# Kernel optimization log

Measured on AMD Instinct MI355X. Metric: run time of the kernel, lower is better.

## Reference

```python
import jax, jax.numpy as jnp
import numpy as np

TAU = 0.07        # temperature from init_kwargs
EPS = 1e-8        # torch F.cosine_similarity eps
NEG_INF = -1e9    # mask fill value used by the original module


def setup_inputs() -> dict:
    key = jax.random.key(0)
    k1, k2 = jax.random.split(key)
    B, D = 4096, 512
    anchor = jax.random.normal(k1, (B, D), dtype=jnp.float32)
    positive = jax.random.normal(k2, (B, D), dtype=jnp.float32)
    return {"anchor": anchor, "positive": positive}


def reference(anchor, positive):
    B = anchor.shape[0]
    N = 2 * B
    emb = jnp.concatenate([anchor, positive], axis=0)          # (2B, D)
    # cosine similarity matrix == normalized dot products (same math as the
    # broadcasted F.cosine_similarity, without the O(N^2 D) intermediate)
    norm = jnp.maximum(jnp.linalg.norm(emb, axis=1, keepdims=True), EPS)
    z = emb / norm
    sim = jnp.matmul(z, z.T) / TAU                             # (2B, 2B)

    idx = jnp.arange(N)
    pos_idx = (idx + B) % N                                    # positive pair index
    pos_logits = sim[idx, pos_idx][:, None]                    # (2B, 1)

    # negatives: everything except self and the positive pair
    neg_mask = (
        jnp.ones((N, N), dtype=bool)
        .at[idx, idx].set(False)
        .at[idx, pos_idx].set(False)
    )
    neg_logits = jnp.where(neg_mask, sim, NEG_INF)             # (2B, 2B)

    all_logits = jnp.concatenate([pos_logits, neg_logits], axis=1)  # (2B, 2B+1)
    loss_per_sample = -pos_logits[:, 0] + jax.scipy.special.logsumexp(all_logits, axis=1)
    # every row has a positive, so valid_samples is all-True; reduction='mean'
    return loss_per_sample.mean()
```

## Files before the change

### kernel.cpp

```cpp
#include <hip/hip_runtime.h>
#include <hip/hip_bf16.h>
#include <stdint.h>


#define N_TOT   8192
#define B_HALF  4096
#define DDIM    512
#define INV_TAU 14.285714285714286f
#define TTILES  32
#define NKT     16

typedef __bf16 bf16x8 __attribute__((ext_vector_type(8)));
typedef __bf16 bf16x4 __attribute__((ext_vector_type(4)));
typedef float  floatx4 __attribute__((ext_vector_type(4)));

__device__ __forceinline__ void gl2lds16(const void* g, void* l) {
    __builtin_amdgcn_global_load_lds(
        (const __attribute__((address_space(1))) void*)g,
        (__attribute__((address_space(3))) void*)l, 16, 0, 0);
}

#define S_BARRIER() asm volatile("s_barrier" ::: "memory")
#define LGKM0()     do { asm volatile("s_waitcnt lgkmcnt(0)" ::: "memory"); \
                         __builtin_amdgcn_sched_barrier(0); } while (0)
#define VMCNT4()    asm volatile("s_waitcnt vmcnt(4)" ::: "memory")
#define VMCNT0()    asm volatile("s_waitcnt vmcnt(0)" ::: "memory")
#define VM_NONE()   do {} while (0)

__global__ __launch_bounds__(256) void knorm(const float* __restrict__ anchor,
                                             const float* __restrict__ positive,
                                             __bf16* __restrict__ z,
                                             float* __restrict__ row_sums,
                                             float* __restrict__ out) {
    const int row  = blockIdx.x * 4 + (threadIdx.x >> 6);
    const int lane = threadIdx.x & 63;
    if (lane == 0) row_sums[row] = 0.0f;
    if (blockIdx.x == 0 && threadIdx.x == 0) out[0] = 0.0f;
    const float* src = (row < B_HALF) ? (anchor + (size_t)row * DDIM)
                                      : (positive + (size_t)(row - B_HALF) * DDIM);
    float4 v0 = ((const float4*)src)[lane];
    float4 v1 = ((const float4*)src)[lane + 64];
    float ss = v0.x*v0.x + v0.y*v0.y + v0.z*v0.z + v0.w*v0.w
             + v1.x*v1.x + v1.y*v1.y + v1.z*v1.z + v1.w*v1.w;
    #pragma unroll
    for (int m = 1; m < 64; m <<= 1) ss += __shfl_xor(ss, m, 64);
    const float inv = 1.0f / fmaxf(sqrtf(ss), 1e-8f);
    bf16x4 o0, o1;
    o0[0] = (__bf16)(v0.x*inv); o0[1] = (__bf16)(v0.y*inv);
    o0[2] = (__bf16)(v0.z*inv); o0[3] = (__bf16)(v0.w*inv);
    o1[0] = (__bf16)(v1.x*inv); o1[1] = (__bf16)(v1.y*inv);
    o1[2] = (__bf16)(v1.z*inv); o1[3] = (__bf16)(v1.w*inv);
    bf16x4* dst = (bf16x4*)(z + (size_t)row * DDIM);
    dst[lane]      = o0;
    dst[lane + 64] = o1;
}

__global__ __launch_bounds__(512, 2) void ksim(const __bf16* __restrict__ z,
                                               float* __restrict__ row_sums,
                                               float* __restrict__ pos_sims) {
    int bid = (int)blockIdx.x;
    bid = (bid & 7) * 66 + (bid >> 3);
    int rem = bid, rt = 0;
    while (rem >= TTILES - rt) { rem -= TTILES - rt; rt++; }
    const int ct = rt + rem;
    const bool diag = (rt == ct);
    const bool posb = (ct == rt + 16);

    const int r0 = rt * 256, c0 = ct * 256;
    const int tid  = threadIdx.x;
    const int w    = tid >> 6, lane = tid & 63;
    const int quad = lane >> 4, nlo = lane & 15;
    const int wr   = w >> 2,   wc  = w & 3;
    const int s4   = (nlo >> 1) & 3;

    __shared__ __align__(16) char smem[4][32768];

    const int schunk = ((lane & 3) ^ ((lane >> 3) & 3)) * 8;
    const __bf16* zA = z + (size_t)(r0 + w * 16 + (lane >> 2)) * DDIM + schunk;
    const __bf16* zB = z + (size_t)(c0 + w * 16 + (lane >> 2)) * DDIM + schunk;

#define STAGE_A(T2) do { char* s_ = smem[(T2) & 3]; const int kb_ = (T2) * 32;   \
        gl2lds16(zA + kb_,              s_ + w * 1024);                          \
        gl2lds16(zA + 128 * DDIM + kb_, s_ + 8192 + w * 1024); } while (0)
#define STAGE_B(T2) do { char* s_ = smem[(T2) & 3]; const int kb_ = (T2) * 32;   \
        gl2lds16(zB + kb_,              s_ + 16384 + w * 1024);                  \
        gl2lds16(zB + 128 * DDIM + kb_, s_ + 16384 + 8192 + w * 1024); } while (0)

    floatx4 acc[8][4];
    #pragma unroll
    for (int a = 0; a < 8; a++)
        #pragma unroll
        for (int b = 0; b < 4; b++) acc[a][b] = (floatx4){0.f, 0.f, 0.f, 0.f};

    STAGE_A(0); STAGE_B(0);
    STAGE_A(1); STAGE_B(1);
    VMCNT4();
    S_BARRIER();

#define KTILE(T, DO_STAGE, VMW) do {                                                  \
        char* As_ = smem[(T) & 3];                                                    \
        char* Bs_ = As_ + 16384;                                                      \
        bf16x8 af[4], bfr[4];                                                         \
                                                    \
        _Pragma("unroll") for (int mi = 0; mi < 4; mi++)                              \
            af[mi] = *(const bf16x8*)(As_ + (wr * 128 + mi * 16 + nlo) * 64           \
                                          + ((quad ^ s4) * 16));                      \
        _Pragma("unroll") for (int ni = 0; ni < 4; ni++)                              \
            bfr[ni] = *(const bf16x8*)(Bs_ + (wc * 64 + ni * 16 + nlo) * 64           \
                                           + ((quad ^ s4) * 16));                     \
        if (DO_STAGE) STAGE_A((T) + 2);                                               \
        S_BARRIER(); LGKM0();                                                         \
        __builtin_amdgcn_s_setprio(1);                                                \
        _Pragma("unroll") for (int mi = 0; mi < 4; mi++)                              \
            _Pragma("unroll") for (int ni = 0; ni < 4; ni++)                          \
                acc[mi][ni] = __builtin_amdgcn_mfma_f32_16x16x32_bf16(                \
                    af[mi], bfr[ni], acc[mi][ni], 0, 0, 0);                           \
        __builtin_amdgcn_s_setprio(0);                                                \
        S_BARRIER();                                                                  \
                           \
        _Pragma("unroll") for (int mi = 0; mi < 4; mi++)                              \
            af[mi] = *(const bf16x8*)(As_ + (wr * 128 + 64 + mi * 16 + nlo) * 64      \
                                          + ((quad ^ s4) * 16));                      \
        if (DO_STAGE) STAGE_B((T) + 2);                                               \
        S_BARRIER(); LGKM0();                                                         \
        __builtin_amdgcn_s_setprio(1);                                                \
        _Pragma("unroll") for (int mi = 0; mi < 4; mi++)                              \
            _Pragma("unroll") for (int ni = 0; ni < 4; ni++)                          \
                acc[4 + mi][ni] = __builtin_amdgcn_mfma_f32_16x16x32_bf16(            \
                    af[mi], bfr[ni], acc[4 + mi][ni], 0, 0, 0);                       \
        __builtin_amdgcn_s_setprio(0);                                                \
        VMW();                                                                        \
        S_BARRIER();                                                                  \
    } while (0)

    for (int t = 0; t < NKT - 2; ++t) KTILE(t, true, VMCNT4);
    KTILE(NKT - 2, false, VMCNT0);
    KTILE(NKT - 1, false, VM_NONE);

    __syncthreads();
    float* rbuf = (float*)smem;
    float* cbuf = (float*)(smem[0] + 4096);

    float cs[4] = {0.f, 0.f, 0.f, 0.f};
    #pragma unroll
    for (int mi = 0; mi < 8; mi++) {
        #pragma unroll
        for (int reg = 0; reg < 4; reg++) {
            const int il = wr * 128 + mi * 16 + quad * 4 + reg;
            const int i  = r0 + il;
            const int ipos = i ^ B_HALF;
            float rs = 0.f;
            #pragma unroll
            for (int ni = 0; ni < 4; ni++) {
                const int j = c0 + wc * 64 + ni * 16 + nlo;
                const float sim = acc[mi][ni][reg] * INV_TAU;
                float e = __expf(sim - INV_TAU);
                if (diag && j == i) e = 0.f;
                if (posb && j == ipos) {
                    pos_sims[i] = sim;
                    pos_sims[j] = sim;
                }
                rs += e;
                cs[ni] += e;
            }
            rs += __shfl_xor(rs, 1, 64);
            rs += __shfl_xor(rs, 2, 64);
            rs += __shfl_xor(rs, 4, 64);
            rs += __shfl_xor(rs, 8, 64);
            if (nlo == 0) rbuf[il * 4 + wc] = rs;
        }
    }
    if (!diag) {
        #pragma unroll
        for (int ni = 0; ni < 4; ni++) {
            float c = cs[ni];
            c += __shfl_xor(c, 16, 64);
            c += __shfl_xor(c, 32, 64);
            if (quad == 0) cbuf[(wc * 64 + ni * 16 + nlo) * 2 + wr] = c;
        }
    }
    __syncthreads();
    if (tid < 256) {
        const float s = rbuf[tid * 4] + rbuf[tid * 4 + 1]
                      + rbuf[tid * 4 + 2] + rbuf[tid * 4 + 3];
        atomicAdd(&row_sums[r0 + tid], s);
    } else if (!diag) {
        const int c = tid - 256;
        atomicAdd(&row_sums[c0 + c], cbuf[c * 2] + cbuf[c * 2 + 1]);
    }
#undef KTILE
#undef STAGE_A
#undef STAGE_B
}

__global__ __launch_bounds__(256) void kfinal(const float* __restrict__ row_sums,
                                              const float* __restrict__ pos_sims,
                                              float* __restrict__ out) {
    const int r = blockIdx.x * 256 + threadIdx.x;
    float v = INV_TAU + __logf(row_sums[r]) - pos_sims[r];
    #pragma unroll
    for (int m = 1; m < 64; m <<= 1) v += __shfl_xor(v, m, 64);
    __shared__ float wsum[4];
    if ((threadIdx.x & 63) == 0) wsum[threadIdx.x >> 6] = v;
    __syncthreads();
    if (threadIdx.x == 0)
        atomicAdd(out, (wsum[0] + wsum[1] + wsum[2] + wsum[3]) * (1.0f / (float)N_TOT));
}

extern "C" void kernel_launch(void* const* d_in, const int* in_sizes, int n_in,
                              void* d_out, int out_size, void* d_ws, size_t ws_size,
                              hipStream_t stream) {
    const float* anchor   = (const float*)d_in[0];
    const float* positive = (const float*)d_in[1];
    float* out = (float*)d_out;

    char* ws = (char*)d_ws;
    __bf16* z        = (__bf16*)ws;
    float*  row_sums = (float*)(ws + 8388608);
    float*  pos_sims = (float*)(ws + 8388608 + 32768);

    knorm<<<N_TOT / 4, 256, 0, stream>>>(anchor, positive, z, row_sums, out);
    ksim<<<528, 512, 0, stream>>>(z, row_sums, pos_sims);
    kfinal<<<N_TOT / 256, 256, 0, stream>>>(row_sums, pos_sims, out);
}
```

Baseline: 137.5 us.

## Double-buffer LDS fragments, deepen prefetch, and fuse final reduction via last-block counter

Restructures the GEMM main loop to prefetch the next k-tile's A/B register fragments while the current MFMAs run, using partial lgkmcnt waits and one barrier per tile instead of several, and staging three tiles ahead in the 4-slot LDS ring. It also removes the separate kfinal launch by having the last finishing ksim block, detected with an atomic done counter, compute the log-sum loss reduction. This cuts barrier stalls and one kernel launch, at the cost of more register pressure from the extra fragment buffers and a serial final reduction in one block.

```diff
diff --git a/kernel.cpp b/kernel.cpp
--- a/kernel.cpp
+++ b/kernel.cpp
@@ -21,8 +21,6 @@
 }
 
 #define S_BARRIER() asm volatile("s_barrier" ::: "memory")
-#define LGKM0()     do { asm volatile("s_waitcnt lgkmcnt(0)" ::: "memory"); \
-                         __builtin_amdgcn_sched_barrier(0); } while (0)
 #define VMCNT4()    asm volatile("s_waitcnt vmcnt(4)" ::: "memory")
 #define VMCNT0()    asm volatile("s_waitcnt vmcnt(0)" ::: "memory")
 #define VM_NONE()   do {} while (0)
@@ -31,11 +29,11 @@
                                              const float* __restrict__ positive,
                                              __bf16* __restrict__ z,
                                              float* __restrict__ row_sums,
-                                             float* __restrict__ out) {
+                                             unsigned* __restrict__ done_ctr) {
     const int row  = blockIdx.x * 4 + (threadIdx.x >> 6);
     const int lane = threadIdx.x & 63;
     if (lane == 0) row_sums[row] = 0.0f;
-    if (blockIdx.x == 0 && threadIdx.x == 0) out[0] = 0.0f;
+    if (blockIdx.x == 0 && threadIdx.x == 0) *done_ctr = 0u;
     const float* src = (row < B_HALF) ? (anchor + (size_t)row * DDIM)
                                       : (positive + (size_t)(row - B_HALF) * DDIM);
     float4 v0 = ((const float4*)src)[lane];
@@ -57,7 +55,9 @@
 
 __global__ __launch_bounds__(512, 2) void ksim(const __bf16* __restrict__ z,
                                                float* __restrict__ row_sums,
-                                               float* __restrict__ pos_sims) {
+                                               float* __restrict__ pos_sims,
+                                               unsigned* __restrict__ done_ctr,
+                                               float* __restrict__ out) {
     int bid = (int)blockIdx.x;
     bid = (bid & 7) * 66 + (bid >> 3);
     int rem = bid, rt = 0;
@@ -74,6 +74,8 @@
     const int s4   = (nlo >> 1) & 3;
 
     __shared__ __align__(16) char smem[4][32768];
+    __shared__ unsigned lastf;
+    __shared__ float fsum[8];
 
     const int schunk = ((lane & 3) ^ ((lane >> 3) & 3)) * 8;
     const __bf16* zA = z + (size_t)(r0 + w * 16 + (lane >> 2)) * DDIM + schunk;
@@ -92,50 +94,73 @@
         #pragma unroll
         for (int b = 0; b < 4; b++) acc[a][b] = (floatx4){0.f, 0.f, 0.f, 0.f};
 
+    bf16x8 afX[4], afY[4], afH[4], bfX[4], bfY[4];
+    const char* smb = (const char*)smem;
+    const int xo   = (quad ^ s4) * 16;
+    const int aoff = (wr * 128 + nlo) * 64 + xo;
+    const int boff = 16384 + (wc * 64 + nlo) * 64 + xo;
+
     STAGE_A(0); STAGE_B(0);
     STAGE_A(1); STAGE_B(1);
+    STAGE_A(2); STAGE_B(2);
     VMCNT4();
     S_BARRIER();
-
-#define KTILE(T, DO_STAGE, VMW) do {                                                  \
-        char* As_ = smem[(T) & 3];                                                    \
-        char* Bs_ = As_ + 16384;                                                      \
-        bf16x8 af[4], bfr[4];                                                         \
-                                                    \
-        _Pragma("unroll") for (int mi = 0; mi < 4; mi++)                              \
-            af[mi] = *(const bf16x8*)(As_ + (wr * 128 + mi * 16 + nlo) * 64           \
-                                          + ((quad ^ s4) * 16));                      \
-        _Pragma("unroll") for (int ni = 0; ni < 4; ni++)                              \
-            bfr[ni] = *(const bf16x8*)(Bs_ + (wc * 64 + ni * 16 + nlo) * 64           \
-                                           + ((quad ^ s4) * 16));                     \
-        if (DO_STAGE) STAGE_A((T) + 2);                                               \
-        S_BARRIER(); LGKM0();                                                         \
-        __builtin_amdgcn_s_setprio(1);                                                \
-        _Pragma("unroll") for (int mi = 0; mi < 4; mi++)                              \
-            _Pragma("unroll") for (int ni = 0; ni < 4; ni++)                          \
-                acc[mi][ni] = __builtin_amdgcn_mfma_f32_16x16x32_bf16(                \
-                    af[mi], bfr[ni], acc[mi][ni], 0, 0, 0);                           \
-        __builtin_amdgcn_s_setprio(0);                                                \
-        S_BARRIER();                                                                  \
-                           \
-        _Pragma("unroll") for (int mi = 0; mi < 4; mi++)                              \
-            af[mi] = *(const bf16x8*)(As_ + (wr * 128 + 64 + mi * 16 + nlo) * 64      \
-                                          + ((quad ^ s4) * 16));                      \
-        if (DO_STAGE) STAGE_B((T) + 2);                                               \
-        S_BARRIER(); LGKM0();                                                         \
-        __builtin_amdgcn_s_setprio(1);                                                \
-        _Pragma("unroll") for (int mi = 0; mi < 4; mi++)                              \
-            _Pragma("unroll") for (int ni = 0; ni < 4; ni++)                          \
-                acc[4 + mi][ni] = __builtin_amdgcn_mfma_f32_16x16x32_bf16(            \
-                    af[mi], bfr[ni], acc[4 + mi][ni], 0, 0, 0);                       \
-        __builtin_amdgcn_s_setprio(0);                                                \
-        VMW();                                                                        \
-        S_BARRIER();                                                                  \
+    #pragma unroll
+    for (int mi = 0; mi < 4; mi++)
+        afX[mi] = *(const bf16x8*)(smb + aoff + mi * 1024);
+    #pragma unroll
+    for (int ni = 0; ni < 4; ni++)
+        bfX[ni] = *(const bf16x8*)(smb + boff + ni * 1024);
+
+#define TILE(T, AC, AN, BC, BN, DO_STAGE, ISSUE_NEXT, VMW) do {                        \
+        const int sl_ = ((T) & 3) * 32768, sn_ = (((T) + 1) & 3) * 32768;              \
+        _Pragma("unroll") for (int mi = 0; mi < 4; mi++)                               \
+            afH[mi] = *(const bf16x8*)(smb + sl_ + aoff + 4096 + mi * 1024);           \
+        if (DO_STAGE) { STAGE_A((T) + 3); }                                            \
+        asm volatile("s_waitcnt lgkmcnt(4)" ::: "memory");                             \
+        __builtin_amdgcn_sched_barrier(0);                                             \
+        __builtin_amdgcn_s_setprio(1);                                                 \
+        _Pragma("unroll") for (int mi = 0; mi < 4; mi++)                               \
+            _Pragma("unroll") for (int ni = 0; ni < 4; ni++)                           \
+                acc[mi][ni] = __builtin_amdgcn_mfma_f32_16x16x32_bf16(                 \
+                    AC[mi], BC[ni], acc[mi][ni], 0, 0, 0);                             \
+        __builtin_amdgcn_s_setprio(0);                                                 \
+        if (ISSUE_NEXT) {                                                              \
+            _Pragma("unroll") for (int mi = 0; mi < 4; mi++)                           \
+                AN[mi] = *(const bf16x8*)(smb + sn_ + aoff + mi * 1024);               \
+            _Pragma("unroll") for (int ni = 0; ni < 4; ni++)                           \
+                BN[ni] = *(const bf16x8*)(smb + sn_ + boff + ni * 1024);               \
+        }                                                                              \
+        if (DO_STAGE) { STAGE_B((T) + 3); }                                            \
+        if (ISSUE_NEXT) { asm volatile("s_waitcnt lgkmcnt(8)" ::: "memory"); }         \
+        else            { asm volatile("s_waitcnt lgkmcnt(0)" ::: "memory"); }         \
+        __builtin_amdgcn_sched_barrier(0);                                             \
+        __builtin_amdgcn_s_setprio(1);                                                 \
+        _Pragma("unroll") for (int mi = 0; mi < 4; mi++)                               \
+            _Pragma("unroll") for (int ni = 0; ni < 4; ni++)                           \
+                acc[4 + mi][ni] = __builtin_amdgcn_mfma_f32_16x16x32_bf16(             \
+                    afH[mi], BC[ni], acc[4 + mi][ni], 0, 0, 0);                        \
+        __builtin_amdgcn_s_setprio(0);                                                 \
+        VMW();                                                                         \
+        S_BARRIER();                                                                   \
     } while (0)
 
-    for (int t = 0; t < NKT - 2; ++t) KTILE(t, true, VMCNT4);
-    KTILE(NKT - 2, false, VMCNT0);
-    KTILE(NKT - 1, false, VM_NONE);
+    TILE( 0, afX, afY, bfX, bfY, 1, 1, VMCNT4);
+    TILE( 1, afY, afX, bfY, bfX, 1, 1, VMCNT4);
+    TILE( 2, afX, afY, bfX, bfY, 1, 1, VMCNT4);
+    TILE( 3, afY, afX, bfY, bfX, 1, 1, VMCNT4);
+    TILE( 4, afX, afY, bfX, bfY, 1, 1, VMCNT4);
+    TILE( 5, afY, afX, bfY, bfX, 1, 1, VMCNT4);
+    TILE( 6, afX, afY, bfX, bfY, 1, 1, VMCNT4);
+    TILE( 7, afY, afX, bfY, bfX, 1, 1, VMCNT4);
+    TILE( 8, afX, afY, bfX, bfY, 1, 1, VMCNT4);
+    TILE( 9, afY, afX, bfY, bfX, 1, 1, VMCNT4);
+    TILE(10, afX, afY, bfX, bfY, 1, 1, VMCNT4);
+    TILE(11, afY, afX, bfY, bfX, 1, 1, VMCNT4);
+    TILE(12, afX, afY, bfX, bfY, 1, 1, VMCNT4);
+    TILE(13, afY, afX, bfY, bfX, 0, 1, VMCNT0);
+    TILE(14, afX, afY, bfX, bfY, 0, 1, VM_NONE);
+    TILE(15, afY, afX, bfY, bfX, 0, 0, VM_NONE);
 
     __syncthreads();
     float* rbuf = (float*)smem;
@@ -188,23 +213,28 @@
         const int c = tid - 256;
         atomicAdd(&row_sums[c0 + c], cbuf[c * 2] + cbuf[c * 2 + 1]);
     }
-#undef KTILE
+
+    __threadfence();
+    __syncthreads();
+    if (tid == 0) lastf = (atomicAdd(done_ctr, 1u) == 527u) ? 1u : 0u;
+    __syncthreads();
+    if (!lastf) return;
+    __threadfence();
+    float a = 0.f;
+    for (int i = tid; i < N_TOT; i += 512)
+        a += INV_TAU + __logf(row_sums[i]) - pos_sims[i];
+    #pragma unroll
+    for (int m = 1; m < 64; m <<= 1) a += __shfl_xor(a, m, 64);
+    if (lane == 0) fsum[w] = a;
+    __syncthreads();
+    if (tid == 0) {
+        float t = fsum[0] + fsum[1] + fsum[2] + fsum[3]
+                + fsum[4] + fsum[5] + fsum[6] + fsum[7];
+        out[0] = t * (1.0f / (float)N_TOT);
+    }
+#undef TILE
 #undef STAGE_A
 #undef STAGE_B
-}
-
-__global__ __launch_bounds__(256) void kfinal(const float* __restrict__ row_sums,
-                                              const float* __restrict__ pos_sims,
-                                              float* __restrict__ out) {
-    const int r = blockIdx.x * 256 + threadIdx.x;
-    float v = INV_TAU + __logf(row_sums[r]) - pos_sims[r];
-    #pragma unroll
-    for (int m = 1; m < 64; m <<= 1) v += __shfl_xor(v, m, 64);
-    __shared__ float wsum[4];
-    if ((threadIdx.x & 63) == 0) wsum[threadIdx.x >> 6] = v;
-    __syncthreads();
-    if (threadIdx.x == 0)
-        atomicAdd(out, (wsum[0] + wsum[1] + wsum[2] + wsum[3]) * (1.0f / (float)N_TOT));
 }
 
 extern "C" void kernel_launch(void* const* d_in, const int* in_sizes, int n_in,
@@ -218,8 +248,8 @@
     __bf16* z        = (__bf16*)ws;
     float*  row_sums = (float*)(ws + 8388608);
     float*  pos_sims = (float*)(ws + 8388608 + 32768);
-
-    knorm<<<N_TOT / 4, 256, 0, stream>>>(anchor, positive, z, row_sums, out);
-    ksim<<<528, 512, 0, stream>>>(z, row_sums, pos_sims);
-    kfinal<<<N_TOT / 256, 256, 0, stream>>>(row_sums, pos_sims, out);
-}
+    unsigned* done_ctr = (unsigned*)(ws + 8388608 + 65536);
+
+    knorm<<<N_TOT / 4, 256, 0, stream>>>(anchor, positive, z, row_sums, done_ctr);
+    ksim<<<528, 512, 0, stream>>>(z, row_sums, pos_sims, done_ctr, out);
+}
```

Result: slower. 200.3 us (+45.6%).

## Replace LDS-pipelined 256x256 sim tiles with direct-global-load 128x128 tiles

Applied to the files above, without the earlier changes.

The similarity kernel drops the LDS staging pipeline (global_load_lds, barriers, swizzle) and has each wave read MFMA operands straight from global memory. Output tiles shrink from 256x256 to 128x128 on 4-wave blocks, so the launch grows from 528 to 2080 blocks. Per-row and per-column partial sums are now atomically added from each wave rather than reduced in shared memory first. The aim is to cut synchronization overhead and improve load balance. The cost is losing LDS data reuse, which raises global/L2 traffic, plus many more atomics.

```diff
diff --git a/kernel.cpp b/kernel.cpp
--- a/kernel.cpp
+++ b/kernel.cpp
@@ -7,25 +7,11 @@
 #define B_HALF  4096
 #define DDIM    512
 #define INV_TAU 14.285714285714286f
-#define TTILES  32
-#define NKT     16
+#define TTILES  64
 
 typedef __bf16 bf16x8 __attribute__((ext_vector_type(8)));
 typedef __bf16 bf16x4 __attribute__((ext_vector_type(4)));
 typedef float  floatx4 __attribute__((ext_vector_type(4)));
-
-__device__ __forceinline__ void gl2lds16(const void* g, void* l) {
-    __builtin_amdgcn_global_load_lds(
-        (const __attribute__((address_space(1))) void*)g,
-        (__attribute__((address_space(3))) void*)l, 16, 0, 0);
-}
-
-#define S_BARRIER() asm volatile("s_barrier" ::: "memory")
-#define LGKM0()     do { asm volatile("s_waitcnt lgkmcnt(0)" ::: "memory"); \
-                         __builtin_amdgcn_sched_barrier(0); } while (0)
-#define VMCNT4()    asm volatile("s_waitcnt vmcnt(4)" ::: "memory")
-#define VMCNT0()    asm volatile("s_waitcnt vmcnt(0)" ::: "memory")
-#define VM_NONE()   do {} while (0)
 
 __global__ __launch_bounds__(256) void knorm(const float* __restrict__ anchor,
                                              const float* __restrict__ positive,
@@ -55,142 +41,106 @@
     dst[lane + 64] = o1;
 }
 
-__global__ __launch_bounds__(512, 2) void ksim(const __bf16* __restrict__ z,
+__global__ __launch_bounds__(256, 3) void ksim(const __bf16* __restrict__ z,
                                                float* __restrict__ row_sums,
                                                float* __restrict__ pos_sims) {
     int bid = (int)blockIdx.x;
-    bid = (bid & 7) * 66 + (bid >> 3);
+    bid = (bid & 7) * 260 + (bid >> 3);
     int rem = bid, rt = 0;
     while (rem >= TTILES - rt) { rem -= TTILES - rt; rt++; }
     const int ct = rt + rem;
     const bool diag = (rt == ct);
-    const bool posb = (ct == rt + 16);
+    const bool posb = (ct == rt + 32);
 
-    const int r0 = rt * 256, c0 = ct * 256;
+    const int r0 = rt * 128, c0 = ct * 128;
     const int tid  = threadIdx.x;
     const int w    = tid >> 6, lane = tid & 63;
     const int quad = lane >> 4, nlo = lane & 15;
-    const int wr   = w >> 2,   wc  = w & 3;
-    const int s4   = (nlo >> 1) & 3;
+    const int wrow = (w >> 1) * 64, wcol = (w & 1) * 64;
 
-    __shared__ __align__(16) char smem[4][32768];
+    const __bf16* pa = z + (size_t)(r0 + wrow + nlo) * DDIM + quad * 8;
+    const __bf16* pb = z + (size_t)(c0 + wcol + nlo) * DDIM + quad * 8;
 
-    const int schunk = ((lane & 3) ^ ((lane >> 3) & 3)) * 8;
-    const __bf16* zA = z + (size_t)(r0 + w * 16 + (lane >> 2)) * DDIM + schunk;
-    const __bf16* zB = z + (size_t)(c0 + w * 16 + (lane >> 2)) * DDIM + schunk;
-
-#define STAGE_A(T2) do { char* s_ = smem[(T2) & 3]; const int kb_ = (T2) * 32;   \
-        gl2lds16(zA + kb_,              s_ + w * 1024);                          \
-        gl2lds16(zA + 128 * DDIM + kb_, s_ + 8192 + w * 1024); } while (0)
-#define STAGE_B(T2) do { char* s_ = smem[(T2) & 3]; const int kb_ = (T2) * 32;   \
-        gl2lds16(zB + kb_,              s_ + 16384 + w * 1024);                  \
-        gl2lds16(zB + 128 * DDIM + kb_, s_ + 16384 + 8192 + w * 1024); } while (0)
-
-    floatx4 acc[8][4];
+    floatx4 acc[4][4];
     #pragma unroll
-    for (int a = 0; a < 8; a++)
+    for (int a = 0; a < 4; a++)
         #pragma unroll
         for (int b = 0; b < 4; b++) acc[a][b] = (floatx4){0.f, 0.f, 0.f, 0.f};
 
-    STAGE_A(0); STAGE_B(0);
-    STAGE_A(1); STAGE_B(1);
-    VMCNT4();
-    S_BARRIER();
+    #pragma unroll 4
+    for (int kt = 0; kt < 16; kt++) {
+        bf16x8 af[4], bfr[4];
+        #pragma unroll
+        for (int mi = 0; mi < 4; mi++)
+            af[mi] = *(const bf16x8*)(pa + mi * 16 * DDIM + kt * 32);
+        #pragma unroll
+        for (int ni = 0; ni < 4; ni++)
+            bfr[ni] = *(const bf16x8*)(pb + ni * 16 * DDIM + kt * 32);
+        #pragma unroll
+        for (int mi = 0; mi < 4; mi++)
+            #pragma unroll
+            for (int ni = 0; ni < 4; ni++)
+                acc[mi][ni] = __builtin_amdgcn_mfma_f32_16x16x32_bf16(
+                    af[mi], bfr[ni], acc[mi][ni], 0, 0, 0);
+    }
 
-#define KTILE(T, DO_STAGE, VMW) do {                                                  \
-        char* As_ = smem[(T) & 3];                                                    \
-        char* Bs_ = As_ + 16384;                                                      \
-        bf16x8 af[4], bfr[4];                                                         \
-                                                    \
-        _Pragma("unroll") for (int mi = 0; mi < 4; mi++)                              \
-            af[mi] = *(const bf16x8*)(As_ + (wr * 128 + mi * 16 + nlo) * 64           \
-                                          + ((quad ^ s4) * 16));                      \
-        _Pragma("unroll") for (int ni = 0; ni < 4; ni++)                              \
-            bfr[ni] = *(const bf16x8*)(Bs_ + (wc * 64 + ni * 16 + nlo) * 64           \
-                                           + ((quad ^ s4) * 16));                     \
-        if (DO_STAGE) STAGE_A((T) + 2);                                               \
-        S_BARRIER(); LGKM0();                                                         \
-        __builtin_amdgcn_s_setprio(1);                                                \
-        _Pragma("unroll") for (int mi = 0; mi < 4; mi++)                              \
-            _Pragma("unroll") for (int ni = 0; ni < 4; ni++)                          \
-                acc[mi][ni] = __builtin_amdgcn_mfma_f32_16x16x32_bf16(                \
-                    af[mi], bfr[ni], acc[mi][ni], 0, 0, 0);                           \
-        __builtin_amdgcn_s_setprio(0);                                                \
-        S_BARRIER();                                                                  \
-                           \
-        _Pragma("unroll") for (int mi = 0; mi < 4; mi++)                              \
-            af[mi] = *(const bf16x8*)(As_ + (wr * 128 + 64 + mi * 16 + nlo) * 64      \
-                                          + ((quad ^ s4) * 16));                      \
-        if (DO_STAGE) STAGE_B((T) + 2);                                               \
-        S_BARRIER(); LGKM0();                                                         \
-        __builtin_amdgcn_s_setprio(1);                                                \
-        _Pragma("unroll") for (int mi = 0; mi < 4; mi++)                              \
-            _Pragma("unroll") for (int ni = 0; ni < 4; ni++)                          \
-                acc[4 + mi][ni] = __builtin_amdgcn_mfma_f32_16x16x32_bf16(            \
-                    af[mi], bfr[ni], acc[4 + mi][ni], 0, 0, 0);                       \
-        __builtin_amdgcn_s_setprio(0);                                                \
-        VMW();                                                                        \
-        S_BARRIER();                                                                  \
-    } while (0)
-
-    for (int t = 0; t < NKT - 2; ++t) KTILE(t, true, VMCNT4);
-    KTILE(NKT - 2, false, VMCNT0);
-    KTILE(NKT - 1, false, VM_NONE);
-
-    __syncthreads();
-    float* rbuf = (float*)smem;
-    float* cbuf = (float*)(smem[0] + 4096);
-
-    float cs[4] = {0.f, 0.f, 0.f, 0.f};
-    #pragma unroll
-    for (int mi = 0; mi < 8; mi++) {
+    if (diag) {
         #pragma unroll
-        for (int reg = 0; reg < 4; reg++) {
-            const int il = wr * 128 + mi * 16 + quad * 4 + reg;
-            const int i  = r0 + il;
-            const int ipos = i ^ B_HALF;
-            float rs = 0.f;
+        for (int mi = 0; mi < 4; mi++) {
             #pragma unroll
-            for (int ni = 0; ni < 4; ni++) {
-                const int j = c0 + wc * 64 + ni * 16 + nlo;
-                const float sim = acc[mi][ni][reg] * INV_TAU;
-                float e = __expf(sim - INV_TAU);
-                if (diag && j == i) e = 0.f;
-                if (posb && j == ipos) {
-                    pos_sims[i] = sim;
-                    pos_sims[j] = sim;
+            for (int reg = 0; reg < 4; reg++) {
+                const int i = r0 + wrow + mi * 16 + quad * 4 + reg;
+                float rs = 0.f;
+                #pragma unroll
+                for (int ni = 0; ni < 4; ni++) {
+                    const int j = c0 + wcol + ni * 16 + nlo;
+                    const float e = __expf(acc[mi][ni][reg] * INV_TAU - INV_TAU);
+                    rs += (j == i) ? 0.f : e;
                 }
-                rs += e;
-                cs[ni] += e;
+                rs += __shfl_xor(rs, 1, 64);
+                rs += __shfl_xor(rs, 2, 64);
+                rs += __shfl_xor(rs, 4, 64);
+                rs += __shfl_xor(rs, 8, 64);
+                if (nlo == 0) atomicAdd(&row_sums[i], rs);
             }
-            rs += __shfl_xor(rs, 1, 64);
-            rs += __shfl_xor(rs, 2, 64);
-            rs += __shfl_xor(rs, 4, 64);
-            rs += __shfl_xor(rs, 8, 64);
-            if (nlo == 0) rbuf[il * 4 + wc] = rs;
         }
-    }
-    if (!diag) {
+    } else {
+        float cs[4] = {0.f, 0.f, 0.f, 0.f};
+        #pragma unroll
+        for (int mi = 0; mi < 4; mi++) {
+            #pragma unroll
+            for (int reg = 0; reg < 4; reg++) {
+                const int i = r0 + wrow + mi * 16 + quad * 4 + reg;
+                const int ipos = i ^ B_HALF;
+                float rs = 0.f;
+                #pragma unroll
+                for (int ni = 0; ni < 4; ni++) {
+                    const int j = c0 + wcol + ni * 16 + nlo;
+                    const float sim = acc[mi][ni][reg] * INV_TAU;
+                    const float e = __expf(sim - INV_TAU);
+                    if (posb && j == ipos) {
+                        pos_sims[i] = sim;
+                        pos_sims[j] = sim;
+                    }
+                    rs += e;
+                    cs[ni] += e;
+                }
+                rs += __shfl_xor(rs, 1, 64);
+                rs += __shfl_xor(rs, 2, 64);
+                rs += __shfl_xor(rs, 4, 64);
+                rs += __shfl_xor(rs, 8, 64);
+                if (nlo == 0) atomicAdd(&row_sums[i], rs);
+            }
+        }
         #pragma unroll
         for (int ni = 0; ni < 4; ni++) {
             float c = cs[ni];
             c += __shfl_xor(c, 16, 64);
             c += __shfl_xor(c, 32, 64);
-            if (quad == 0) cbuf[(wc * 64 + ni * 16 + nlo) * 2 + wr] = c;
+            if (quad == 0)
+                atomicAdd(&row_sums[c0 + wcol + ni * 16 + nlo], c);
         }
     }
-    __syncthreads();
-    if (tid < 256) {
-        const float s = rbuf[tid * 4] + rbuf[tid * 4 + 1]
-                      + rbuf[tid * 4 + 2] + rbuf[tid * 4 + 3];
-        atomicAdd(&row_sums[r0 + tid], s);
-    } else if (!diag) {
-        const int c = tid - 256;
-        atomicAdd(&row_sums[c0 + c], cbuf[c * 2] + cbuf[c * 2 + 1]);
-    }
-#undef KTILE
-#undef STAGE_A
-#undef STAGE_B
 }
 
 __global__ __launch_bounds__(256) void kfinal(const float* __restrict__ row_sums,
@@ -220,6 +170,6 @@
     float*  pos_sims = (float*)(ws + 8388608 + 32768);
 
     knorm<<<N_TOT / 4, 256, 0, stream>>>(anchor, positive, z, row_sums, out);
-    ksim<<<528, 512, 0, stream>>>(z, row_sums, pos_sims);
+    ksim<<<2080, 256, 0, stream>>>(z, row_sums, pos_sims);
     kfinal<<<N_TOT / 256, 256, 0, stream>>>(row_sums, pos_sims, out);
 }
```

Result: slower. 214.0 us (+55.6%).
